# Optimization experiments

Measured on AMD Instinct MI355X. Metric: run time of the kernel, lower is better.

## Reference

```python
import jax, jax.numpy as jnp
import numpy as np

L, N, E = 2048, 2, 512
H = 8
HD = E // H
FF = 2048
NLAYERS = 2
EPS = 1e-5


def setup_inputs() -> dict:
    key = jax.random.key(0)
    ks = jax.random.split(key, 8)
    s = 0.02
    return {
        "src": jax.random.normal(ks[0], (L, N, E), jnp.float32),
        # packed qkv projection, torch Linear convention: y = x @ W.T + b
        "in_proj_w": jax.random.normal(ks[1], (NLAYERS, 3 * E, E), jnp.float32) * s,
        "in_proj_b": jnp.zeros((NLAYERS, 3 * E), jnp.float32),
        "out_proj_w": jax.random.normal(ks[2], (NLAYERS, E, E), jnp.float32) * s,
        "out_proj_b": jnp.zeros((NLAYERS, E), jnp.float32),
        "lin1_w": jax.random.normal(ks[3], (NLAYERS, FF, E), jnp.float32) * s,
        "lin1_b": jnp.zeros((NLAYERS, FF), jnp.float32),
        "lin2_w": jax.random.normal(ks[4], (NLAYERS, E, FF), jnp.float32) * s,
        "lin2_b": jnp.zeros((NLAYERS, E), jnp.float32),
        "ln1_g": jnp.ones((NLAYERS, E), jnp.float32),
        "ln1_b": jnp.zeros((NLAYERS, E), jnp.float32),
        "ln2_g": jnp.ones((NLAYERS, E), jnp.float32),
        "ln2_b": jnp.zeros((NLAYERS, E), jnp.float32),
    }


def _layer_norm(x, g, b):
    mu = jnp.mean(x, axis=-1, keepdims=True)
    var = jnp.mean(jnp.square(x - mu), axis=-1, keepdims=True)
    return (x - mu) * jax.lax.rsqrt(var + EPS) * g + b


def _mha(x, w_qkv, b_qkv, w_o, b_o):
    # x: [L, N, E] (seq-first, as in torch multi_head_attention_forward)
    qkv = jnp.einsum('lne,fe->lnf', x, w_qkv) + b_qkv  # [L, N, 3E]
    q, k, v = jnp.split(qkv, 3, axis=-1)
    q = q.reshape(L, N, H, HD) * (1.0 / np.sqrt(HD))  # torch scales q pre-bmm
    k = k.reshape(L, N, H, HD)
    v = v.reshape(L, N, H, HD)
    scores = jnp.einsum('lnhd,snhd->nhls', q, k)  # [N, H, L, S] -- O(L*S) matrix
    attn = jax.nn.softmax(scores, axis=-1)
    o = jnp.einsum('nhls,snhd->lnhd', attn, v).reshape(L, N, E)
    return jnp.einsum('lne,fe->lnf', o, w_o) + b_o


def reference(src, in_proj_w, in_proj_b, out_proj_w, out_proj_b,
              lin1_w, lin1_b, lin2_w, lin2_b, ln1_g, ln1_b, ln2_g, ln2_b):
    x = src
    for i in range(NLAYERS):  # fixed small layer count
        a = _mha(x, in_proj_w[i], in_proj_b[i], out_proj_w[i], out_proj_b[i])
        x = _layer_norm(x + a, ln1_g[i], ln1_b[i])  # post-norm (torch default)
        h = jax.nn.relu(jnp.einsum('lne,fe->lnf', x, lin1_w[i]) + lin1_b[i])
        f = jnp.einsum('lnf,ef->lne', h, lin2_w[i]) + lin2_b[i]
        x = _layer_norm(x + f, ln2_g[i], ln2_b[i])
    return x
```

## Files before the change

kernel.cpp:

```cpp
#include <hip/hip_runtime.h>
#include <hip/hip_bf16.h>

using bf16 = __hip_bfloat16;
typedef __bf16 bf16x8 __attribute__((ext_vector_type(8)));
typedef float f32x4 __attribute__((ext_vector_type(4)));

#define MFMA(a, b, c) __builtin_amdgcn_mfma_f32_16x16x32_bf16(a, b, c, 0, 0, 0)

constexpr int L = 2048, N = 2, E = 512, H = 8, HD = 64, FF = 2048;
constexpr int T = L * N;

__global__ void detect_dtype(const unsigned int* __restrict__ g,
                             int* __restrict__ flag) {
  if (threadIdx.x == 0 && blockIdx.x == 0)
    *flag = (g[0] != 0x3F800000u) ? 1 : 0;
}

struct CvtBigArgs {
  const void* src[5];
  bf16* dst[5];
  int n[5];
};
__global__ __launch_bounds__(256) void cvt_big(CvtBigArgs a,
                                               const int* __restrict__ flag) {
  long long idx = (long long)(blockIdx.x * 256 + threadIdx.x) * 8;
  int s = 0;
  while (s < 5 && idx >= a.n[s]) { idx -= a.n[s]; ++s; }
  if (s >= 5) return;
  bf16* dst = a.dst[s];
  if (*flag) {
    *(uint4*)&dst[idx] = *(const uint4*)&((const bf16*)a.src[s])[idx];
  } else {
    const float* src = (const float*)a.src[s];
    float4 x = *(const float4*)&src[idx];
    float4 y = *(const float4*)&src[idx + 4];
    bf16 o8[8] = {__float2bfloat16(x.x), __float2bfloat16(x.y),
                  __float2bfloat16(x.z), __float2bfloat16(x.w),
                  __float2bfloat16(y.x), __float2bfloat16(y.y),
                  __float2bfloat16(y.z), __float2bfloat16(y.w)};
    *(uint4*)&dst[idx] = *(const uint4*)o8;
  }
}

struct CvtParArgs {
  const void* src[8];
  float* dst[8];
  int n[8];
};
__global__ __launch_bounds__(256) void cvt_par(CvtParArgs a,
                                               const int* __restrict__ flag) {
  int idx = blockIdx.x * 256 + threadIdx.x;
  int s = 0;
  while (s < 8 && idx >= a.n[s]) { idx -= a.n[s]; ++s; }
  if (s >= 8) return;
  a.dst[s][idx] = (*flag) ? __bfloat162float(((const bf16*)a.src[s])[idx])
                          : ((const float*)a.src[s])[idx];
}

__device__ __forceinline__ void gload16(const bf16* g, bf16* l) {
  __builtin_amdgcn_global_load_lds(
      (const __attribute__((address_space(1))) unsigned int*)g,
      (__attribute__((address_space(3))) unsigned int*)l, 16, 0, 0);
}

template <bool RELU, int BM, int BN>
__global__ __launch_bounds__(256) void gemm_bt(
    const bf16* __restrict__ A, const bf16* __restrict__ W,
    const float* __restrict__ bias, const bf16* __restrict__ res,
    bf16* __restrict__ C, int M, int F, int K) {
  constexpr int SA = BM / 32;
  constexpr int SB = BN / 32;
  constexpr int MI = BM / 32;
  constexpr int NI = BN / 32;
  __shared__ __align__(16) bf16 As[2][BM * 64];
  __shared__ __align__(16) bf16 Bs[2][BN * 64];
  const int bm = blockIdx.x, bn = blockIdx.y;
  const int tid = threadIdx.x;
  const int w = tid >> 6, lane = tid & 63;
  const int wr = w >> 1, wc = w & 1;
  const int lhi = lane >> 4, llo = lane & 15;
  f32x4 acc[MI][NI] = {};

  const bf16 *ap[SA], *wp[SB];
#pragma unroll
  for (int s = 0; s < SA; ++s) {
    int c = tid + s * 256;
    ap[s] = &A[(size_t)(bm * BM + c % BM) * K + (c / BM) * 8];
  }
#pragma unroll
  for (int s = 0; s < SB; ++s) {
    int c = tid + s * 256;
    wp[s] = &W[(size_t)(bn * BN + c % BN) * K + (c / BN) * 8];
  }
  auto stage = [&](int buf, int k0) {
#pragma unroll
    for (int s = 0; s < SA; ++s)
      gload16(ap[s] + k0, &As[buf][(tid + s * 256) * 8]);
#pragma unroll
    for (int s = 0; s < SB; ++s)
      gload16(wp[s] + k0, &Bs[buf][(tid + s * 256) * 8]);
  };

  stage(0, 0);
  int cur = 0;
  for (int k0 = 0; k0 < K; k0 += 64) {
    __syncthreads();
    if (k0 + 64 < K) stage(cur ^ 1, k0 + 64);
    bf16x8 af[MI][2], bfr[NI][2];
#pragma unroll
    for (int mi = 0; mi < MI; ++mi)
#pragma unroll
      for (int ks = 0; ks < 2; ++ks)
        af[mi][ks] = *(const bf16x8*)&As[cur]
            [((ks * 4 + lhi) * BM + wr * (BM / 2) + mi * 16 + llo) * 8];
#pragma unroll
    for (int ni = 0; ni < NI; ++ni)
#pragma unroll
      for (int ks = 0; ks < 2; ++ks)
        bfr[ni][ks] = *(const bf16x8*)&Bs[cur]
            [((ks * 4 + lhi) * BN + wc * (BN / 2) + ni * 16 + llo) * 8];
    __builtin_amdgcn_s_setprio(1);
#pragma unroll
    for (int ks = 0; ks < 2; ++ks)
#pragma unroll
      for (int mi = 0; mi < MI; ++mi)
#pragma unroll
        for (int ni = 0; ni < NI; ++ni)
          acc[mi][ni] = MFMA(af[mi][ks], bfr[ni][ks], acc[mi][ni]);
    __builtin_amdgcn_s_setprio(0);
    cur ^= 1;
  }
#pragma unroll
  for (int mi = 0; mi < MI; ++mi) {
#pragma unroll
    for (int ni = 0; ni < NI; ++ni) {
      int col = bn * BN + wc * (BN / 2) + ni * 16 + llo;
      float bv = bias[col];
#pragma unroll
      for (int r = 0; r < 4; ++r) {
        int row = bm * BM + wr * (BM / 2) + mi * 16 + lhi * 4 + r;
        float v = acc[mi][ni][r] + bv;
        if (RELU) v = fmaxf(v, 0.f);
        if (res) v += __bfloat162float(res[(size_t)row * F + col]);
        C[(size_t)row * F + col] = __float2bfloat16(v);
      }
    }
  }
}

__global__ __launch_bounds__(256) void prep_kv(
    const bf16* __restrict__ qkv, bf16* __restrict__ kt,
    bf16* __restrict__ vt) {
  __shared__ __align__(16) bf16 Vl[64 * 72];
  const int blk = blockIdx.x;
  const int kb = blk & 31, nh = blk >> 5;
  const int n = nh >> 3, h = nh & 7;
  const int tid = threadIdx.x;
  bf16* ko = kt + ((size_t)nh * 32 + kb) * 4096;
  bf16* vo = vt + ((size_t)nh * 32 + kb) * 4096;
#pragma unroll
  for (int s = 0; s < 2; ++s) {
    int c = tid + s * 256;
    int jj = c >> 3, g = c & 7;
    size_t t = (size_t)((kb * 64 + jj) * N + n);
    uint4 kk = *(const uint4*)&qkv[t * 1536 + 512 + h * 64 + g * 8];
    *(uint4*)&ko[jj * 64 + ((g ^ (jj & 7)) * 8)] = kk;
    uint4 vv = *(const uint4*)&qkv[t * 1536 + 1024 + h * 64 + g * 8];
    *(uint4*)&Vl[jj * 72 + g * 8] = vv;
  }
  __syncthreads();
#pragma unroll
  for (int s = 0; s < 2; ++s) {
    int c = tid + s * 256;
    int d = c >> 3, gsw = c & 7;
    int g = gsw ^ (d & 7);
    bf16 tmp[8];
#pragma unroll
    for (int e = 0; e < 8; ++e) tmp[e] = Vl[(g * 8 + e) * 72 + d];
    *(uint4*)&vo[d * 64 + gsw * 8] = *(const uint4*)tmp;
  }
}

__global__ __launch_bounds__(256) void attn_split(
    const bf16* __restrict__ qkv, const bf16* __restrict__ kt,
    const bf16* __restrict__ vt, bf16* __restrict__ opart,
    float* __restrict__ lpart) {
  __shared__ __align__(16) bf16 Kb[2][4096];
  __shared__ __align__(16) bf16 Vb[2][4096];
  __shared__ __align__(16) bf16 Ps[128 * 72];
  const int blk = blockIdx.x;
  const int rest = blk >> 3;
  const int nh = (blk & 7) * 2 + (rest & 1);
  const int split = (rest >> 1) & 3;
  const int qb = rest >> 3;
  const int n = nh >> 3, h = nh & 7;
  const int tid = threadIdx.x;
  const int w = tid >> 6, lane = tid & 63;
  const int lhi = lane >> 4, llo = lane & 15;
  const int kb0 = split * 8, kb1 = kb0 + 8;

#pragma unroll
  for (int s = 0; s < 4; ++s) {
    int c = tid + s * 256;
    int i = c >> 3, dc = c & 7;
    size_t t = (size_t)((qb * 128 + i) * N + n);
    *(uint4*)&Ps[i * 72 + dc * 8] =
        *(const uint4*)&qkv[t * 1536 + h * 64 + dc * 8];
  }
  __syncthreads();
  bf16x8 aq[2][2];
#pragma unroll
  for (int rg = 0; rg < 2; ++rg)
#pragma unroll
    for (int ks = 0; ks < 2; ++ks)
      aq[rg][ks] = *(const bf16x8*)
          &Ps[(w * 32 + rg * 16 + llo) * 72 + ks * 32 + lhi * 8];

  const bf16* ktile = kt + (size_t)nh * 32 * 4096;
  const bf16* vtile = vt + (size_t)nh * 32 * 4096;
  auto stage = [&](int buf, int kb) {
#pragma unroll
    for (int s = 0; s < 2; ++s) {
      int c = tid + s * 256;
      gload16(ktile + (size_t)kb * 4096 + c * 8, &Kb[buf][c * 8]);
      gload16(vtile + (size_t)kb * 4096 + c * 8, &Vb[buf][c * 8]);
    }
  };
  stage(0, kb0);

  float psum[2][4] = {};
  f32x4 o[2][4] = {};
  int cur = 0;

  for (int kb = kb0; kb < kb1; ++kb) {
    __syncthreads();
    if (kb + 1 < kb1) stage(cur ^ 1, kb + 1);

    f32x4 sfr[2][4] = {};
    __builtin_amdgcn_s_setprio(1);
#pragma unroll
    for (int cb = 0; cb < 4; ++cb) {
      const int row = cb * 16 + llo;
#pragma unroll
      for (int ks = 0; ks < 2; ++ks) {
        bf16x8 b = *(const bf16x8*)&Kb[cur]
            [row * 64 + (((ks * 4 + lhi) ^ (row & 7)) << 3)];
#pragma unroll
        for (int rg = 0; rg < 2; ++rg)
          sfr[rg][cb] = MFMA(aq[rg][ks], b, sfr[rg][cb]);
      }
    }
    __builtin_amdgcn_s_setprio(0);

#pragma unroll
    for (int rg = 0; rg < 2; ++rg)
#pragma unroll
      for (int cb = 0; cb < 4; ++cb)
#pragma unroll
        for (int r = 0; r < 4; ++r) {
          float p = __expf(sfr[rg][cb][r] * 0.125f);
          psum[rg][r] += p;
          Ps[(w * 32 + rg * 16 + lhi * 4 + r) * 72 + cb * 16 + llo] =
              __float2bfloat16(p);
        }
    asm volatile("" ::: "memory");

    __builtin_amdgcn_s_setprio(1);
#pragma unroll
    for (int cb = 0; cb < 4; ++cb) {
      const int crow = cb * 16 + llo;
#pragma unroll
      for (int ks = 0; ks < 2; ++ks) {
        bf16x8 b = *(const bf16x8*)&Vb[cur]
            [crow * 64 + (((ks * 4 + lhi) ^ (crow & 7)) << 3)];
#pragma unroll
        for (int rg = 0; rg < 2; ++rg) {
          bf16x8 a = *(const bf16x8*)
              &Ps[(w * 32 + rg * 16 + llo) * 72 + ks * 32 + lhi * 8];
          o[rg][cb] = MFMA(a, b, o[rg][cb]);
        }
      }
    }
    __builtin_amdgcn_s_setprio(0);
    cur ^= 1;
  }

#pragma unroll
  for (int rg = 0; rg < 2; ++rg)
#pragma unroll
    for (int r = 0; r < 4; ++r) {
      float v = psum[rg][r];
#pragma unroll
      for (int d = 1; d < 16; d <<= 1) v += __shfl_xor(v, d);
      psum[rg][r] = v;
    }
#pragma unroll
  for (int rg = 0; rg < 2; ++rg)
#pragma unroll
    for (int cb = 0; cb < 4; ++cb)
#pragma unroll
      for (int r = 0; r < 4; ++r) {
        int i = w * 32 + rg * 16 + lhi * 4 + r;
        int d = cb * 16 + llo;
        size_t t = (size_t)((qb * 128 + i) * N + n);
        opart[((size_t)split * T + t) * E + h * 64 + d] =
            __float2bfloat16(o[rg][cb][r]);
      }
  if (llo == 0) {
#pragma unroll
    for (int rg = 0; rg < 2; ++rg)
#pragma unroll
      for (int r = 0; r < 4; ++r) {
        int i = w * 32 + rg * 16 + lhi * 4 + r;
        size_t t = (size_t)((qb * 128 + i) * N + n);
        lpart[(size_t)(split * T + t) * H + h] = psum[rg][r];
      }
  }
}

__global__ __launch_bounds__(256) void attn_merge(
    const bf16* __restrict__ opart, const float* __restrict__ lpart,
    bf16* __restrict__ atn) {
  int i = (blockIdx.x * 256 + threadIdx.x) * 8;
  if (i >= T * E) return;
  int t = i >> 9, h = (i >> 6) & 7;
  float l = 0.f, acc[8] = {};
#pragma unroll
  for (int s = 0; s < 4; ++s) {
    l += lpart[(size_t)(s * T + t) * H + h];
    uint4 v = *(const uint4*)&opart[(size_t)s * T * E + i];
    const bf16* e8 = (const bf16*)&v;
#pragma unroll
    for (int e = 0; e < 8; ++e) acc[e] += __bfloat162float(e8[e]);
  }
  float rl = 1.f / l;
  bf16 r8[8];
#pragma unroll
  for (int e = 0; e < 8; ++e) r8[e] = __float2bfloat16(acc[e] * rl);
  *(uint4*)&atn[i] = *(const uint4*)r8;
}

template <typename OutT>
__global__ __launch_bounds__(256) void ln_one(
    const bf16* __restrict__ y, const float* __restrict__ g,
    const float* __restrict__ b, OutT* __restrict__ out) {
  const int t = blockIdx.x;
  const int tid = threadIdx.x;
  const int w = tid >> 6, lane = tid & 63;
  const int e = tid * 2;
  const size_t base = (size_t)t * E;
  float v0 = __bfloat162float(y[base + e]);
  float v1 = __bfloat162float(y[base + e + 1]);
  float s = v0 + v1, q = v0 * v0 + v1 * v1;
#pragma unroll
  for (int d = 1; d < 64; d <<= 1) {
    s += __shfl_xor(s, d);
    q += __shfl_xor(q, d);
  }
  __shared__ float rs[4], rq[4];
  if (lane == 0) { rs[w] = s; rq[w] = q; }
  __syncthreads();
  float S = rs[0] + rs[1] + rs[2] + rs[3];
  float Qq = rq[0] + rq[1] + rq[2] + rq[3];
  float mu = S * (1.f / E);
  float var = Qq * (1.f / E) - mu * mu;
  float rstd = rsqrtf(var + 1e-5f);
  float o0 = (v0 - mu) * rstd * g[e] + b[e];
  float o1 = (v1 - mu) * rstd * g[e + 1] + b[e + 1];
  if constexpr (__is_same(OutT, float)) {
    out[base + e] = o0;
    out[base + e + 1] = o1;
  } else {
    out[base + e] = __float2bfloat16(o0);
    out[base + e + 1] = __float2bfloat16(o1);
  }
}

extern "C" void kernel_launch(void* const* d_in, const int* in_sizes, int n_in,
                              void* d_out, int out_size, void* d_ws,
                              size_t ws_size, hipStream_t stream) {
  int* flag = (int*)d_ws;
  float* pbuf = (float*)((char*)d_ws + 16);
  float* in_b = pbuf;
  float* ob   = in_b + 3072;
  float* l1b  = ob + 1024;
  float* l2b  = l1b + 4096;
  float* ln1g = l2b + 1024;
  float* ln1b = ln1g + 1024;
  float* ln2g = ln1b + 1024;
  float* ln2b = ln2g + 1024;
  bf16* big  = (bf16*)(ln2b + 1024);
  bf16* srcb = big;
  bf16* in_w = srcb + (size_t)T * E;
  bf16* ow   = in_w + (size_t)2 * 1536 * E;
  bf16* l1w  = ow + (size_t)2 * E * E;
  bf16* l2w  = l1w + (size_t)2 * FF * E;
  bf16* qkv  = l2w + (size_t)2 * E * FF;
  bf16* atn  = qkv + (size_t)T * 1536;
  bf16* ybuf = atn + (size_t)T * E;
  bf16* x1   = ybuf + (size_t)T * E;
  bf16* x2   = x1 + (size_t)T * E;
  bf16* hbuf = x2 + (size_t)T * E;
  bf16* ktg  = hbuf + (size_t)T * FF;
  bf16* vtg  = ktg + (size_t)T * E;
  bf16* opart  = hbuf;
  float* lpart = (float*)ybuf;

  detect_dtype<<<1, 64, 0, stream>>>((const unsigned int*)d_in[9], flag);
  CvtBigArgs ba;
  ba.src[0] = d_in[0]; ba.dst[0] = srcb; ba.n[0] = T * E;
  ba.src[1] = d_in[1]; ba.dst[1] = in_w; ba.n[1] = 2 * 1536 * E;
  ba.src[2] = d_in[3]; ba.dst[2] = ow;   ba.n[2] = 2 * E * E;
  ba.src[3] = d_in[5]; ba.dst[3] = l1w;  ba.n[3] = 2 * FF * E;
  ba.src[4] = d_in[7]; ba.dst[4] = l2w;  ba.n[4] = 2 * E * FF;
  int btot = ba.n[0] + ba.n[1] + ba.n[2] + ba.n[3] + ba.n[4];
  cvt_big<<<dim3(btot / 2048), 256, 0, stream>>>(ba, flag);
  CvtParArgs pa;
  pa.src[0] = d_in[2];  pa.dst[0] = in_b; pa.n[0] = 3072;
  pa.src[1] = d_in[4];  pa.dst[1] = ob;   pa.n[1] = 1024;
  pa.src[2] = d_in[6];  pa.dst[2] = l1b;  pa.n[2] = 4096;
  pa.src[3] = d_in[8];  pa.dst[3] = l2b;  pa.n[3] = 1024;
  pa.src[4] = d_in[9];  pa.dst[4] = ln1g; pa.n[4] = 1024;
  pa.src[5] = d_in[10]; pa.dst[5] = ln1b; pa.n[5] = 1024;
  pa.src[6] = d_in[11]; pa.dst[6] = ln2g; pa.n[6] = 1024;
  pa.src[7] = d_in[12]; pa.dst[7] = ln2b; pa.n[7] = 1024;
  int ptot = 3072 + 1024 + 4096 + 1024 + 1024 * 4;
  cvt_par<<<dim3(ptot / 256), 256, 0, stream>>>(pa, flag);

  const bf16* x = srcb;
  for (int i = 0; i < 2; ++i) {
    gemm_bt<false, 128, 128><<<dim3(T / 128, 1536 / 128), 256, 0, stream>>>(
        x, in_w + (size_t)i * 1536 * E, in_b + i * 1536, nullptr, qkv,
        T, 1536, E);
    prep_kv<<<dim3(512), 256, 0, stream>>>(qkv, ktg, vtg);
    attn_split<<<dim3(1024), 256, 0, stream>>>(qkv, ktg, vtg, opart, lpart);
    attn_merge<<<dim3(T * E / 2048), 256, 0, stream>>>(opart, lpart, atn);
    gemm_bt<false, 64, 64><<<dim3(T / 64, E / 64), 256, 0, stream>>>(
        atn, ow + (size_t)i * E * E, ob + i * E, x, ybuf, T, E, E);
    ln_one<bf16><<<dim3(T), 256, 0, stream>>>(
        ybuf, ln1g + i * E, ln1b + i * E, x1);
    gemm_bt<true, 128, 128><<<dim3(T / 128, FF / 128), 256, 0, stream>>>(
        x1, l1w + (size_t)i * FF * E, l1b + i * FF, nullptr, hbuf,
        T, FF, E);
    gemm_bt<false, 64, 64><<<dim3(T / 64, E / 64), 256, 0, stream>>>(
        hbuf, l2w + (size_t)i * E * FF, l2b + i * E, x1, ybuf, T, E, FF);
    if (i == 1) {
      ln_one<float><<<dim3(T), 256, 0, stream>>>(
          ybuf, ln2g + i * E, ln2b + i * E, (float*)d_out);
    } else {
      ln_one<bf16><<<dim3(T), 256, 0, stream>>>(
          ybuf, ln2g + i * E, ln2b + i * E, x2);
    }
    x = x2;
  }
}
```

Baseline: 320.2 us.

## Fuse K/V transpose into QKV GEMM epilogue and split-merge into out-proj GEMM

The QKV projection GEMM now writes K and V directly into the swizzled, transposed per-head block layouts that attention consumes, which removes the separate prep_kv kernel and its extra pass over K/V. The out-projection GEMM now loads the four split-attention partial outputs, sums them, normalizes by the summed row sums while staging its A tile, and drops the attn_merge kernel and its intermediate buffer. This saves two launches and two round trips through memory per layer. In exchange the epilogue does scattered scalar stores for K/V, and the out-proj A staging becomes synchronous global loads plus arithmetic instead of async copies.

```diff
diff --git a/kernel.cpp b/kernel.cpp
--- a/kernel.cpp
+++ b/kernel.cpp
@@ -148,36 +148,90 @@
   }
 }
 
-__global__ __launch_bounds__(256) void prep_kv(
-    const bf16* __restrict__ qkv, bf16* __restrict__ kt,
-    bf16* __restrict__ vt) {
-  __shared__ __align__(16) bf16 Vl[64 * 72];
-  const int blk = blockIdx.x;
-  const int kb = blk & 31, nh = blk >> 5;
-  const int n = nh >> 3, h = nh & 7;
+__global__ __launch_bounds__(256) void gemm_qkv(
+    const bf16* __restrict__ A, const bf16* __restrict__ W,
+    const float* __restrict__ bias, bf16* __restrict__ qkv,
+    bf16* __restrict__ kt, bf16* __restrict__ vt) {
+  constexpr int BM = 128, BN = 128, K = E;
+  __shared__ __align__(16) bf16 As[2][BM * 64];
+  __shared__ __align__(16) bf16 Bs[2][BN * 64];
+  const int bm = blockIdx.x, bn = blockIdx.y;
   const int tid = threadIdx.x;
-  bf16* ko = kt + ((size_t)nh * 32 + kb) * 4096;
-  bf16* vo = vt + ((size_t)nh * 32 + kb) * 4096;
-#pragma unroll
-  for (int s = 0; s < 2; ++s) {
+  const int w = tid >> 6, lane = tid & 63;
+  const int wr = w >> 1, wc = w & 1;
+  const int lhi = lane >> 4, llo = lane & 15;
+  f32x4 acc[4][4] = {};
+
+  const bf16 *ap[4], *wp[4];
+#pragma unroll
+  for (int s = 0; s < 4; ++s) {
     int c = tid + s * 256;
-    int jj = c >> 3, g = c & 7;
-    size_t t = (size_t)((kb * 64 + jj) * N + n);
-    uint4 kk = *(const uint4*)&qkv[t * 1536 + 512 + h * 64 + g * 8];
-    *(uint4*)&ko[jj * 64 + ((g ^ (jj & 7)) * 8)] = kk;
-    uint4 vv = *(const uint4*)&qkv[t * 1536 + 1024 + h * 64 + g * 8];
-    *(uint4*)&Vl[jj * 72 + g * 8] = vv;
-  }
-  __syncthreads();
-#pragma unroll
-  for (int s = 0; s < 2; ++s) {
-    int c = tid + s * 256;
-    int d = c >> 3, gsw = c & 7;
-    int g = gsw ^ (d & 7);
-    bf16 tmp[8];
-#pragma unroll
-    for (int e = 0; e < 8; ++e) tmp[e] = Vl[(g * 8 + e) * 72 + d];
-    *(uint4*)&vo[d * 64 + gsw * 8] = *(const uint4*)tmp;
+    ap[s] = &A[(size_t)(bm * BM + c % BM) * K + (c / BM) * 8];
+    wp[s] = &W[(size_t)(bn * BN + c % BN) * K + (c / BN) * 8];
+  }
+  auto stage = [&](int buf, int k0) {
+#pragma unroll
+    for (int s = 0; s < 4; ++s) {
+      gload16(ap[s] + k0, &As[buf][(tid + s * 256) * 8]);
+      gload16(wp[s] + k0, &Bs[buf][(tid + s * 256) * 8]);
+    }
+  };
+
+  stage(0, 0);
+  int cur = 0;
+  for (int k0 = 0; k0 < K; k0 += 64) {
+    __syncthreads();
+    if (k0 + 64 < K) stage(cur ^ 1, k0 + 64);
+    bf16x8 af[4][2], bfr[4][2];
+#pragma unroll
+    for (int mi = 0; mi < 4; ++mi)
+#pragma unroll
+      for (int ks = 0; ks < 2; ++ks)
+        af[mi][ks] = *(const bf16x8*)&As[cur]
+            [((ks * 4 + lhi) * BM + wr * 64 + mi * 16 + llo) * 8];
+#pragma unroll
+    for (int ni = 0; ni < 4; ++ni)
+#pragma unroll
+      for (int ks = 0; ks < 2; ++ks)
+        bfr[ni][ks] = *(const bf16x8*)&Bs[cur]
+            [((ks * 4 + lhi) * BN + wc * 64 + ni * 16 + llo) * 8];
+    __builtin_amdgcn_s_setprio(1);
+#pragma unroll
+    for (int ks = 0; ks < 2; ++ks)
+#pragma unroll
+      for (int mi = 0; mi < 4; ++mi)
+#pragma unroll
+        for (int ni = 0; ni < 4; ++ni)
+          acc[mi][ni] = MFMA(af[mi][ks], bfr[ni][ks], acc[mi][ni]);
+    __builtin_amdgcn_s_setprio(0);
+    cur ^= 1;
+  }
+#pragma unroll
+  for (int mi = 0; mi < 4; ++mi) {
+#pragma unroll
+    for (int ni = 0; ni < 4; ++ni) {
+      int col = bn * BN + wc * 64 + ni * 16 + llo;
+      float bv = bias[col];
+#pragma unroll
+      for (int r = 0; r < 4; ++r) {
+        int row = bm * BM + wr * 64 + mi * 16 + lhi * 4 + r;
+        float v = acc[mi][ni][r] + bv;
+        int n_ = row & 1, jj = (row >> 1) & 63;
+        if (col < 512) {
+          qkv[(size_t)row * 1536 + col] = __float2bfloat16(v);
+        } else if (col < 1024) {
+          int h = (col - 512) >> 6, d = (col - 512) & 63;
+          int g = d >> 3, e = d & 7;
+          kt[(size_t)((n_ * 8 + h) * 32 + bm) * 4096 + jj * 64 +
+             ((g ^ (jj & 7)) << 3) + e] = __float2bfloat16(v);
+        } else {
+          int h = (col - 1024) >> 6, d = (col - 1024) & 63;
+          int gv = jj >> 3, ev = jj & 7;
+          vt[(size_t)((n_ * 8 + h) * 32 + bm) * 4096 + d * 64 +
+             ((gv ^ (d & 7)) << 3) + ev] = __float2bfloat16(v);
+        }
+      }
+    }
   }
 }
 
@@ -318,26 +372,100 @@
   }
 }
 
-__global__ __launch_bounds__(256) void attn_merge(
+__global__ __launch_bounds__(256) void gemm_out(
     const bf16* __restrict__ opart, const float* __restrict__ lpart,
-    bf16* __restrict__ atn) {
-  int i = (blockIdx.x * 256 + threadIdx.x) * 8;
-  if (i >= T * E) return;
-  int t = i >> 9, h = (i >> 6) & 7;
-  float l = 0.f, acc[8] = {};
-#pragma unroll
-  for (int s = 0; s < 4; ++s) {
-    l += lpart[(size_t)(s * T + t) * H + h];
-    uint4 v = *(const uint4*)&opart[(size_t)s * T * E + i];
-    const bf16* e8 = (const bf16*)&v;
-#pragma unroll
-    for (int e = 0; e < 8; ++e) acc[e] += __bfloat162float(e8[e]);
-  }
-  float rl = 1.f / l;
-  bf16 r8[8];
-#pragma unroll
-  for (int e = 0; e < 8; ++e) r8[e] = __float2bfloat16(acc[e] * rl);
-  *(uint4*)&atn[i] = *(const uint4*)r8;
+    const bf16* __restrict__ W, const float* __restrict__ bias,
+    const bf16* __restrict__ res, bf16* __restrict__ C) {
+  __shared__ __align__(16) bf16 As[2][64 * 64];
+  __shared__ __align__(16) bf16 Bs[2][64 * 64];
+  const int bm = blockIdx.x, bn = blockIdx.y;
+  const int tid = threadIdx.x;
+  const int w = tid >> 6, lane = tid & 63;
+  const int wr = w >> 1, wc = w & 1;
+  const int lhi = lane >> 4, llo = lane & 15;
+  f32x4 acc[2][2] = {};
+
+  const bf16* wp[2];
+#pragma unroll
+  for (int s = 0; s < 2; ++s) {
+    int c = tid + s * 256;
+    wp[s] = &W[(size_t)(bn * 64 + (c & 63)) * E + (c >> 6) * 8];
+  }
+  const int arow = bm * 64 + (tid & 63);
+  const int kg0 = tid >> 6;
+
+  auto stage = [&](int buf, int kk) {
+#pragma unroll
+    for (int s = 0; s < 2; ++s)
+      gload16(wp[s] + kk * 64, &Bs[buf][(tid + s * 256) * 8]);
+    float lsum = 0.f;
+#pragma unroll
+    for (int sp = 0; sp < 4; ++sp)
+      lsum += lpart[(size_t)(sp * T + arow) * H + kk];
+    float rl = 1.f / lsum;
+#pragma unroll
+    for (int s = 0; s < 2; ++s) {
+      int kg = kg0 + s * 4;
+      float a8[8] = {};
+#pragma unroll
+      for (int sp = 0; sp < 4; ++sp) {
+        uint4 v = *(const uint4*)
+            &opart[((size_t)sp * T + arow) * E + kk * 64 + kg * 8];
+        const bf16* e8 = (const bf16*)&v;
+#pragma unroll
+        for (int e = 0; e < 8; ++e) a8[e] += __bfloat162float(e8[e]);
+      }
+      bf16 o8[8];
+#pragma unroll
+      for (int e = 0; e < 8; ++e) o8[e] = __float2bfloat16(a8[e] * rl);
+      *(uint4*)&As[buf][(kg * 64 + (tid & 63)) * 8] = *(const uint4*)o8;
+    }
+  };
+
+  stage(0, 0);
+  int cur = 0;
+  for (int kk = 0; kk < 8; ++kk) {
+    __syncthreads();
+    if (kk + 1 < 8) stage(cur ^ 1, kk + 1);
+    bf16x8 af[2][2], bfr[2][2];
+#pragma unroll
+    for (int mi = 0; mi < 2; ++mi)
+#pragma unroll
+      for (int ks = 0; ks < 2; ++ks)
+        af[mi][ks] = *(const bf16x8*)&As[cur]
+            [((ks * 4 + lhi) * 64 + wr * 32 + mi * 16 + llo) * 8];
+#pragma unroll
+    for (int ni = 0; ni < 2; ++ni)
+#pragma unroll
+      for (int ks = 0; ks < 2; ++ks)
+        bfr[ni][ks] = *(const bf16x8*)&Bs[cur]
+            [((ks * 4 + lhi) * 64 + wc * 32 + ni * 16 + llo) * 8];
+    __builtin_amdgcn_s_setprio(1);
+#pragma unroll
+    for (int ks = 0; ks < 2; ++ks)
+#pragma unroll
+      for (int mi = 0; mi < 2; ++mi)
+#pragma unroll
+        for (int ni = 0; ni < 2; ++ni)
+          acc[mi][ni] = MFMA(af[mi][ks], bfr[ni][ks], acc[mi][ni]);
+    __builtin_amdgcn_s_setprio(0);
+    cur ^= 1;
+  }
+#pragma unroll
+  for (int mi = 0; mi < 2; ++mi) {
+#pragma unroll
+    for (int ni = 0; ni < 2; ++ni) {
+      int col = bn * 64 + wc * 32 + ni * 16 + llo;
+      float bv = bias[col];
+#pragma unroll
+      for (int r = 0; r < 4; ++r) {
+        int row = bm * 64 + wr * 32 + mi * 16 + lhi * 4 + r;
+        float v = acc[mi][ni][r] + bv +
+                  __bfloat162float(res[(size_t)row * E + col]);
+        C[(size_t)row * E + col] = __float2bfloat16(v);
+      }
+    }
+  }
 }
 
 template <typename OutT>
@@ -404,7 +532,7 @@
   bf16* ktg  = hbuf + (size_t)T * FF;
   bf16* vtg  = ktg + (size_t)T * E;
   bf16* opart  = hbuf;
-  float* lpart = (float*)ybuf;
+  float* lpart = (float*)atn;
 
   detect_dtype<<<1, 64, 0, stream>>>((const unsigned int*)d_in[9], flag);
   CvtBigArgs ba;
@@ -429,14 +557,11 @@
 
   const bf16* x = srcb;
   for (int i = 0; i < 2; ++i) {
-    gemm_bt<false, 128, 128><<<dim3(T / 128, 1536 / 128), 256, 0, stream>>>(
-        x, in_w + (size_t)i * 1536 * E, in_b + i * 1536, nullptr, qkv,
-        T, 1536, E);
-    prep_kv<<<dim3(512), 256, 0, stream>>>(qkv, ktg, vtg);
+    gemm_qkv<<<dim3(T / 128, 1536 / 128), 256, 0, stream>>>(
+        x, in_w + (size_t)i * 1536 * E, in_b + i * 1536, qkv, ktg, vtg);
     attn_split<<<dim3(1024), 256, 0, stream>>>(qkv, ktg, vtg, opart, lpart);
-    attn_merge<<<dim3(T * E / 2048), 256, 0, stream>>>(opart, lpart, atn);
-    gemm_bt<false, 64, 64><<<dim3(T / 64, E / 64), 256, 0, stream>>>(
-        atn, ow + (size_t)i * E * E, ob + i * E, x, ybuf, T, E, E);
+    gemm_out<<<dim3(T / 64, E / 64), 256, 0, stream>>>(
+        opart, lpart, ow + (size_t)i * E * E, ob + i * E, x, ybuf);
     ln_one<bf16><<<dim3(T), 256, 0, stream>>>(
         ybuf, ln1g + i * E, ln1b + i * E, x1);
     gemm_bt<true, 128, 128><<<dim3(T / 128, FF / 128), 256, 0, stream>>>(
```

Measured after the change: 347.0 us. 1.08x slower.

## Split-K the FFN down-projection and fuse partial reduction into LayerNorm

Applied to the files above, without the earlier changes.

Replaces the FF2 GEMM (K=2048, only 512 output tiles) with a two-way split-K kernel that writes fp32 partials into the idle qkv buffer. The following LayerNorm kernel sums the two partials and adds bias and residual before normalizing. This doubles the number of blocks to fill the GPU better on a long-K GEMM, at the cost of extra fp32 partial traffic. It also removes the separate bf16 rounding of the pre-norm sum.

```diff
diff --git a/kernel.cpp b/kernel.cpp
--- a/kernel.cpp
+++ b/kernel.cpp
@@ -148,6 +148,77 @@
   }
 }
 
+__global__ __launch_bounds__(256) void gemm_ff2_split(
+    const bf16* __restrict__ A, const bf16* __restrict__ W,
+    float* __restrict__ part) {
+  constexpr int BM = 64, BN = 64, K = FF, KH = FF / 2;
+  __shared__ __align__(16) bf16 As[2][BM * 64];
+  __shared__ __align__(16) bf16 Bs[2][BN * 64];
+  const int bm = blockIdx.x, bn = blockIdx.y, sp = blockIdx.z;
+  const int koff = sp * KH;
+  const int tid = threadIdx.x;
+  const int w = tid >> 6, lane = tid & 63;
+  const int wr = w >> 1, wc = w & 1;
+  const int lhi = lane >> 4, llo = lane & 15;
+  f32x4 acc[2][2] = {};
+
+  const bf16 *ap[2], *wp[2];
+#pragma unroll
+  for (int s = 0; s < 2; ++s) {
+    int c = tid + s * 256;
+    ap[s] = &A[(size_t)(bm * BM + c % BM) * K + (c / BM) * 8 + koff];
+    wp[s] = &W[(size_t)(bn * BN + c % BN) * K + (c / BN) * 8 + koff];
+  }
+  auto stage = [&](int buf, int k0) {
+#pragma unroll
+    for (int s = 0; s < 2; ++s) {
+      gload16(ap[s] + k0, &As[buf][(tid + s * 256) * 8]);
+      gload16(wp[s] + k0, &Bs[buf][(tid + s * 256) * 8]);
+    }
+  };
+
+  stage(0, 0);
+  int cur = 0;
+  for (int k0 = 0; k0 < KH; k0 += 64) {
+    __syncthreads();
+    if (k0 + 64 < KH) stage(cur ^ 1, k0 + 64);
+    bf16x8 af[2][2], bfr[2][2];
+#pragma unroll
+    for (int mi = 0; mi < 2; ++mi)
+#pragma unroll
+      for (int ks = 0; ks < 2; ++ks)
+        af[mi][ks] = *(const bf16x8*)&As[cur]
+            [((ks * 4 + lhi) * BM + wr * 32 + mi * 16 + llo) * 8];
+#pragma unroll
+    for (int ni = 0; ni < 2; ++ni)
+#pragma unroll
+      for (int ks = 0; ks < 2; ++ks)
+        bfr[ni][ks] = *(const bf16x8*)&Bs[cur]
+            [((ks * 4 + lhi) * BN + wc * 32 + ni * 16 + llo) * 8];
+    __builtin_amdgcn_s_setprio(1);
+#pragma unroll
+    for (int ks = 0; ks < 2; ++ks)
+#pragma unroll
+      for (int mi = 0; mi < 2; ++mi)
+#pragma unroll
+        for (int ni = 0; ni < 2; ++ni)
+          acc[mi][ni] = MFMA(af[mi][ks], bfr[ni][ks], acc[mi][ni]);
+    __builtin_amdgcn_s_setprio(0);
+    cur ^= 1;
+  }
+#pragma unroll
+  for (int mi = 0; mi < 2; ++mi)
+#pragma unroll
+    for (int ni = 0; ni < 2; ++ni) {
+      int col = bn * BN + wc * 32 + ni * 16 + llo;
+#pragma unroll
+      for (int r = 0; r < 4; ++r) {
+        int row = bm * BM + wr * 32 + mi * 16 + lhi * 4 + r;
+        part[(size_t)sp * T * E + (size_t)row * E + col] = acc[mi][ni][r];
+      }
+    }
+}
+
 __global__ __launch_bounds__(256) void prep_kv(
     const bf16* __restrict__ qkv, bf16* __restrict__ kt,
     bf16* __restrict__ vt) {
@@ -351,6 +422,45 @@
   const size_t base = (size_t)t * E;
   float v0 = __bfloat162float(y[base + e]);
   float v1 = __bfloat162float(y[base + e + 1]);
+  float s = v0 + v1, q = v0 * v0 + v1 * v1;
+#pragma unroll
+  for (int d = 1; d < 64; d <<= 1) {
+    s += __shfl_xor(s, d);
+    q += __shfl_xor(q, d);
+  }
+  __shared__ float rs[4], rq[4];
+  if (lane == 0) { rs[w] = s; rq[w] = q; }
+  __syncthreads();
+  float S = rs[0] + rs[1] + rs[2] + rs[3];
+  float Qq = rq[0] + rq[1] + rq[2] + rq[3];
+  float mu = S * (1.f / E);
+  float var = Qq * (1.f / E) - mu * mu;
+  float rstd = rsqrtf(var + 1e-5f);
+  float o0 = (v0 - mu) * rstd * g[e] + b[e];
+  float o1 = (v1 - mu) * rstd * g[e + 1] + b[e + 1];
+  if constexpr (__is_same(OutT, float)) {
+    out[base + e] = o0;
+    out[base + e + 1] = o1;
+  } else {
+    out[base + e] = __float2bfloat16(o0);
+    out[base + e + 1] = __float2bfloat16(o1);
+  }
+}
+
+template <typename OutT>
+__global__ __launch_bounds__(256) void ln_ff2(
+    const float* __restrict__ part, const bf16* __restrict__ res,
+    const float* __restrict__ bias, const float* __restrict__ g,
+    const float* __restrict__ b, OutT* __restrict__ out) {
+  const int t = blockIdx.x;
+  const int tid = threadIdx.x;
+  const int w = tid >> 6, lane = tid & 63;
+  const int e = tid * 2;
+  const size_t base = (size_t)t * E;
+  float v0 = part[base + e] + part[(size_t)T * E + base + e] + bias[e] +
+             __bfloat162float(res[base + e]);
+  float v1 = part[base + e + 1] + part[(size_t)T * E + base + e + 1] +
+             bias[e + 1] + __bfloat162float(res[base + e + 1]);
   float s = v0 + v1, q = v0 * v0 + v1 * v1;
 #pragma unroll
   for (int d = 1; d < 64; d <<= 1) {
@@ -405,6 +515,7 @@
   bf16* vtg  = ktg + (size_t)T * E;
   bf16* opart  = hbuf;
   float* lpart = (float*)ybuf;
+  float* fpart = (float*)qkv;
 
   detect_dtype<<<1, 64, 0, stream>>>((const unsigned int*)d_in[9], flag);
   CvtBigArgs ba;
@@ -442,14 +553,15 @@
     gemm_bt<true, 128, 128><<<dim3(T / 128, FF / 128), 256, 0, stream>>>(
         x1, l1w + (size_t)i * FF * E, l1b + i * FF, nullptr, hbuf,
         T, FF, E);
-    gemm_bt<false, 64, 64><<<dim3(T / 64, E / 64), 256, 0, stream>>>(
-        hbuf, l2w + (size_t)i * E * FF, l2b + i * E, x1, ybuf, T, E, FF);
+    gemm_ff2_split<<<dim3(T / 64, E / 64, 2), 256, 0, stream>>>(
+        hbuf, l2w + (size_t)i * E * FF, fpart);
     if (i == 1) {
-      ln_one<float><<<dim3(T), 256, 0, stream>>>(
-          ybuf, ln2g + i * E, ln2b + i * E, (float*)d_out);
+      ln_ff2<float><<<dim3(T), 256, 0, stream>>>(
+          fpart, x1, l2b + i * E, ln2g + i * E, ln2b + i * E,
+          (float*)d_out);
     } else {
-      ln_one<bf16><<<dim3(T), 256, 0, stream>>>(
-          ybuf, ln2g + i * E, ln2b + i * E, x2);
+      ln_ff2<bf16><<<dim3(T), 256, 0, stream>>>(
+          fpart, x1, l2b + i * E, ln2g + i * E, ln2b + i * E, x2);
     }
     x = x2;
   }
```

Result: no change. 325.2 us (+1.6%).
